# Optimization experiments

Measured on AMD Instinct MI355X. Metric: run time of the kernel, lower is better.

Reference implementation:

```python
import jax, jax.numpy as jnp
import numpy as np

THR = 1.0                      # spike threshold
DECAY_V = float(np.exp(-1.0 / 20.0))
GAMMA = 0.3                    # surrogate-gradient dampening factor
OUT_DECAY = 0.8                # exp_convolve decay

@jax.custom_vjp
def spike_fn(v_scaled):
    # Heaviside spike with pseudo-derivative gamma*max(0, 1-|v_scaled|)
    return (v_scaled > 0.0).astype(v_scaled.dtype)

def _spike_fwd(v_scaled):
    return spike_fn(v_scaled), v_scaled

def _spike_bwd(v_scaled, g):
    return (g * GAMMA * jnp.maximum(0.0, 1.0 - jnp.abs(v_scaled)),)

spike_fn.defvjp(_spike_fwd, _spike_bwd)


def setup_inputs() -> dict:
    key = jax.random.key(0)
    k1, k2, k3, k4 = jax.random.split(key, 4)
    B, T, NI, NR = 32, 1000, 128, 512
    inputs = jax.random.normal(k1, (B, T, NI), dtype=jnp.float32)
    w_in = jax.random.normal(k2, (NI, NR), dtype=jnp.float32) / np.sqrt(NI)
    w_rec = jax.random.normal(k3, (NR, NR), dtype=jnp.float32) / np.sqrt(NR)
    w_out = jax.random.normal(k4, (NR, 1), dtype=jnp.float32) / np.sqrt(NR)
    b_out = jnp.zeros((1,), dtype=jnp.float32)
    return {"inputs": inputs, "w_in": w_in, "w_rec": w_rec, "w_out": w_out, "b_out": b_out}


def reference(inputs, w_in, w_rec, w_out, b_out):
    B, T, _ = inputs.shape
    NR = w_rec.shape[0]
    dtype = inputs.dtype
    # no autapses (zero diagonal on recurrent weights, as in LSNN cells)
    w_rec_masked = w_rec * (1.0 - jnp.eye(NR, dtype=dtype))
    # precompute feedforward input currents: [T, B, NR]
    i_in = jnp.swapaxes(jnp.einsum('bti,iu->btu', inputs, w_in), 0, 1)

    def lif_step(carry, x_t):
        v, z = carry
        i_t = x_t + z @ w_rec_masked           # [B, NR]
        v_new = DECAY_V * v + i_t - z * THR    # reset by subtraction
        z_new = spike_fn((v_new - THR) / THR)
        return (v_new, z_new), (v_new, z_new)

    v0 = jnp.zeros((B, NR), dtype)
    z0 = jnp.zeros((B, NR), dtype)
    _, (vs, zs) = jax.lax.scan(lif_step, (v0, z0), i_in)
    voltages = jnp.swapaxes(vs, 0, 1)  # [B, T, NR]
    spikes = jnp.swapaxes(zs, 0, 1)    # [B, T, NR]

    proj = spikes @ w_out + b_out      # [B, T, 1]

    def filt_step(a, x):
        a_new = OUT_DECAY * a + (1.0 - OUT_DECAY) * x
        return a_new, a_new

    f0 = jnp.zeros((B, 1), dtype)
    _, pred = jax.lax.scan(filt_step, f0, jnp.swapaxes(proj, 0, 1))
    prediction = jnp.swapaxes(pred, 0, 1)  # [B, T, 1]
    return voltages, spikes, prediction
```

## Files before the change

kernel.cpp:

```cpp
#include <hip/hip_runtime.h>

#define NR 512
#define NI 128
#define B 32
#define T 1000
#define G 32

__device__ __forceinline__ float mul_nofma(float a, float b) {
    float r = a * b;
    asm volatile("" : "+v"(r));
    return r;
}

__device__ __forceinline__ void bar_lds() {
    asm volatile("s_waitcnt lgkmcnt(0)\n\ts_barrier" ::: "memory");
}

__global__ __launch_bounds__(512) void k_prep(const float* __restrict__ w_rec,
                                              float* __restrict__ w_ws) {
    const int r = blockIdx.x, u = threadIdx.x;
    float val = 0.f;
    if (r < NR && r != u) val = w_rec[r * NR + u];
    w_ws[r * NR + u] = val;
}

template <int ROWS>
__global__ __launch_bounds__(512) void k_in_gemm(const float* __restrict__ inputs,
                                                 const float* __restrict__ w_in,
                                                 float* __restrict__ i_in) {
    const int u = threadIdx.x;
    const int r0 = blockIdx.x * ROWS;
    float acc[ROWS];
#pragma unroll
    for (int r = 0; r < ROWS; ++r) acc[r] = 0.f;
    const float* __restrict__ inp = inputs + (long)r0 * NI;
#pragma unroll 4
    for (int i = 0; i < NI; ++i) {
        float w = w_in[i * NR + u];
#pragma unroll
        for (int r = 0; r < ROWS; ++r)
            acc[r] = __builtin_fmaf(inp[r * NI + i], w, acc[r]);
    }
#pragma unroll
    for (int r = 0; r < ROWS; ++r)
        i_in[(long)(r0 + r) * NR + u] = acc[r];
}

__device__ __forceinline__ void loadg1(float (&buf)[G], const int* __restrict__ lp,
                                       const float* __restrict__ w_ws, int u) {
#pragma unroll
    for (int qq = 0; qq < G / 4; ++qq) {
        int4 jv = *(const int4*)(lp + qq * 4);
        int j0 = __builtin_amdgcn_readfirstlane(jv.x);
        int j1 = __builtin_amdgcn_readfirstlane(jv.y);
        int j2 = __builtin_amdgcn_readfirstlane(jv.z);
        int j3 = __builtin_amdgcn_readfirstlane(jv.w);
        buf[qq * 4 + 0] = w_ws[j0 * NR + u];
        buf[qq * 4 + 1] = w_ws[j1 * NR + u];
        buf[qq * 4 + 2] = w_ws[j2 * NR + u];
        buf[qq * 4 + 3] = w_ws[j3 * NR + u];
    }
}

__device__ __forceinline__ void sumg1(const float (&buf)[G], float& s) {
#pragma unroll
    for (int q = 0; q < G; ++q) s = __fadd_rn(s, buf[q]);
}

__global__ __launch_bounds__(1024) void k_scan(const float* __restrict__ w_ws,
                                               float* __restrict__ out) {
    const int b = blockIdx.x;
    const int tid = threadIdx.x;
    const int u = tid & (NR - 1);
    const int h = tid >> 9;
    const int wav = tid >> 6;
    const int lane = tid & 63;

    float* __restrict__ volt_b = out + (long)b * (T * NR);
    float* __restrict__ spk_b  = out + (long)B * T * NR + (long)b * (T * NR);

    __shared__ __align__(16) int listA[256];
    __shared__ __align__(16) int listB[256];
    __shared__ int wcnt[8];
    __shared__ float shs[2][NR];

    float v = 0.f, z = 0.f;
    const float decay = 0.951229424500714f;
    __syncthreads();

    for (int t = 0; t < T; ++t) {
        float ii = volt_b[t * NR + u];

        unsigned long long m = __ballot(z > 0.5f);
        if (h == 0 && lane == 0) wcnt[wav] = __popcll(m);
        bar_lds();

        const int c0 = wcnt[0], c1 = wcnt[1], c2 = wcnt[2], c3 = wcnt[3];
        const int c4 = wcnt[4], c5 = wcnt[5], c6 = wcnt[6], c7 = wcnt[7];
        const int cnt_lo = c0 + c1 + c2 + c3;
        const int cnt_hi = c4 + c5 + c6 + c7;

        if (h == 0) {
            if (z > 0.5f) {
                int below = __popcll(m & ((1ull << lane) - 1ull));
                if (wav < 4) {
                    int pos = (wav > 0 ? c0 : 0) + (wav > 1 ? c1 : 0) + (wav > 2 ? c2 : 0) + below;
                    listA[pos] = u;
                } else {
                    int pos = (wav > 4 ? c4 : 0) + (wav > 5 ? c5 : 0) + (wav > 6 ? c6 : 0) + below;
                    listB[pos] = u;
                }
            }
            if (u < 256) { if (u >= cnt_lo) listA[u] = NR; }
            else         { int x = u - 256; if (x >= cnt_hi) listB[x] = NR; }
        }
        bar_lds();

        const int* lp  = h ? listB : listA;
        const int  myn = h ? ((cnt_hi + G - 1) / G) : ((cnt_lo + G - 1) / G);
        float s = 0.f;
        if (myn > 0) {
            float bA[G], bB[G];
            loadg1(bA, lp, w_ws, u);
            int g = 0;
            while (true) {
                if (g + 1 < myn) loadg1(bB, lp + (g + 1) * G, w_ws, u);
                sumg1(bA, s);
                ++g;
                if (g == myn) break;
                if (g + 1 < myn) loadg1(bA, lp + (g + 1) * G, w_ws, u);
                sumg1(bB, s);
                ++g;
                if (g == myn) break;
            }
        }
        shs[h][u] = s;
        bar_lds();

        float rec = __fadd_rn(shs[0][u], shs[1][u]);
        float it = __fadd_rn(ii, rec);
        float m1 = mul_nofma(decay, v);
        float t2 = __fadd_rn(m1, it);
        float vn = __fsub_rn(t2, z);
        float zn = (vn > 1.0f) ? 1.0f : 0.0f;
        if (h == 0) {
            volt_b[t * NR + u] = vn;
            spk_b[t * NR + u]  = zn;
        }
        v = vn; z = zn;
    }
}

__global__ __launch_bounds__(512) void k_pred(const float* __restrict__ w_out,
                                              const float* __restrict__ b_out,
                                              float* __restrict__ out) {
    const int b = blockIdx.x;
    const int tid = threadIdx.x;
    const int wav = tid >> 6, lane = tid & 63;
    const float* __restrict__ spk_b = out + (long)B * T * NR + (long)b * (T * NR);
    float* __restrict__ pred = out + 2L * B * T * NR + (long)b * T;

    __shared__ double projs[T];

    double wo[8];
#pragma unroll
    for (int q = 0; q < 8; ++q) wo[q] = (double)w_out[lane + q * 64];

    for (int t = wav; t < T; t += 8) {
        double p = 0.0;
#pragma unroll
        for (int q = 0; q < 8; ++q)
            p += (double)spk_b[t * NR + lane + q * 64] * wo[q];
#pragma unroll
        for (int o = 32; o > 0; o >>= 1) p += __shfl_xor(p, o, 64);
        if (lane == 0) projs[t] = p;
    }
    __syncthreads();
    if (tid == 0) {
        const double bo = (double)b_out[0];
        double ema = 0.0;
        for (int t = 0; t < T; ++t) {
            ema = 0.8 * ema + 0.2 * (bo + projs[t]);
            pred[t] = (float)ema;
        }
    }
}

__global__ __launch_bounds__(512) void k_scan_ref(const float* __restrict__ w_rec,
                                                  const float* __restrict__ w_out,
                                                  const float* __restrict__ b_out,
                                                  float* __restrict__ out) {
    const int b = blockIdx.x;
    const int u = threadIdx.x;
    const int wav = u >> 6, lane = u & 63;
    const int KC = 256;

    float* __restrict__ volt_b = out + (long)b * (T * NR);
    float* __restrict__ spk_b  = out + (long)B * T * NR + (long)b * (T * NR);
    float* __restrict__ pred   = out + 2L * B * T * NR;

    __shared__ __align__(16) int list[NR];
    __shared__ int wcnt[8];
    __shared__ double projp[8];

    float v = 0.f, z = 0.f;
    const float decay = 0.951229424500714f;
    const double wo = (double)w_out[u];
    const double bo = (double)b_out[0];
    double ema = 0.0;

    for (int t = 0; t < T; ++t) {
        unsigned long long m = __ballot(z > 0.5f);
        if (lane == 0) wcnt[wav] = __popcll(m);
        __syncthreads();
        int cnt = 0, base = 0;
#pragma unroll
        for (int w2 = 0; w2 < 8; ++w2) {
            int c = wcnt[w2];
            if (w2 < wav) base += c;
            cnt += c;
        }
        if (z > 0.5f) {
            int pos = base + __popcll(m & ((1ull << lane) - 1ull));
            list[pos] = u;
        }
        float ii = volt_b[t * NR + u];
        __syncthreads();

        float s1 = 0.f, s2 = 0.f;
        int k = 0;
        for (; k + 8 <= cnt; k += 8) {
            int4 ja = *(const int4*)&list[k];
            int4 jb = *(const int4*)&list[k + 4];
            int j0 = __builtin_amdgcn_readfirstlane(ja.x);
            int j1 = __builtin_amdgcn_readfirstlane(ja.y);
            int j2 = __builtin_amdgcn_readfirstlane(ja.z);
            int j3 = __builtin_amdgcn_readfirstlane(ja.w);
            int j4 = __builtin_amdgcn_readfirstlane(jb.x);
            int j5 = __builtin_amdgcn_readfirstlane(jb.y);
            int j6 = __builtin_amdgcn_readfirstlane(jb.z);
            int j7 = __builtin_amdgcn_readfirstlane(jb.w);
            float w0 = w_rec[j0 * NR + u]; if (j0 == u) w0 = 0.f;
            float w1 = w_rec[j1 * NR + u]; if (j1 == u) w1 = 0.f;
            float w2 = w_rec[j2 * NR + u]; if (j2 == u) w2 = 0.f;
            float w3 = w_rec[j3 * NR + u]; if (j3 == u) w3 = 0.f;
            float w4 = w_rec[j4 * NR + u]; if (j4 == u) w4 = 0.f;
            float w5 = w_rec[j5 * NR + u]; if (j5 == u) w5 = 0.f;
            float w6 = w_rec[j6 * NR + u]; if (j6 == u) w6 = 0.f;
            float w7 = w_rec[j7 * NR + u]; if (j7 == u) w7 = 0.f;
            if (j0 < KC) s1 = __fadd_rn(s1, w0); else s2 = __fadd_rn(s2, w0);
            if (j1 < KC) s1 = __fadd_rn(s1, w1); else s2 = __fadd_rn(s2, w1);
            if (j2 < KC) s1 = __fadd_rn(s1, w2); else s2 = __fadd_rn(s2, w2);
            if (j3 < KC) s1 = __fadd_rn(s1, w3); else s2 = __fadd_rn(s2, w3);
            if (j4 < KC) s1 = __fadd_rn(s1, w4); else s2 = __fadd_rn(s2, w4);
            if (j5 < KC) s1 = __fadd_rn(s1, w5); else s2 = __fadd_rn(s2, w5);
            if (j6 < KC) s1 = __fadd_rn(s1, w6); else s2 = __fadd_rn(s2, w6);
            if (j7 < KC) s1 = __fadd_rn(s1, w7); else s2 = __fadd_rn(s2, w7);
        }
        for (; k < cnt; ++k) {
            int j = __builtin_amdgcn_readfirstlane(list[k]);
            float w = w_rec[j * NR + u];
            if (j == u) w = 0.f;
            if (j < KC) s1 = __fadd_rn(s1, w); else s2 = __fadd_rn(s2, w);
        }
        float rec = __fadd_rn(s1, s2);

        float it = __fadd_rn(ii, rec);
        float m1 = mul_nofma(decay, v);
        float t2 = __fadd_rn(m1, it);
        float vn = __fsub_rn(t2, z);
        float zn = (vn > 1.0f) ? 1.0f : 0.0f;
        volt_b[t * NR + u] = vn;
        spk_b[t * NR + u]  = zn;

        double p = (double)zn * wo;
#pragma unroll
        for (int o = 32; o > 0; o >>= 1) p += __shfl_xor(p, o, 64);
        if (lane == 0) projp[wav] = p;
        __syncthreads();
        if (u == 0) {
            double pr = bo;
#pragma unroll
            for (int w2 = 0; w2 < 8; ++w2) pr += projp[w2];
            ema = 0.8 * ema + 0.2 * pr;
            pred[b * T + t] = (float)ema;
        }
        v = vn; z = zn;
    }
}

extern "C" void kernel_launch(void* const* d_in, const int* in_sizes, int n_in,
                              void* d_out, int out_size, void* d_ws, size_t ws_size,
                              hipStream_t stream) {
    const float* inputs = (const float*)d_in[0];
    const float* w_in   = (const float*)d_in[1];
    const float* w_rec  = (const float*)d_in[2];
    const float* w_out  = (const float*)d_in[3];
    const float* b_out  = (const float*)d_in[4];
    float* out = (float*)d_out;

    k_in_gemm<16><<<dim3(B * T / 16), dim3(512), 0, stream>>>(inputs, w_in, out);

    const size_t need = (size_t)(NR + 1) * NR * sizeof(float);
    if (ws_size >= need) {
        float* w_ws = (float*)d_ws;
        k_prep<<<dim3(NR + 1), dim3(512), 0, stream>>>(w_rec, w_ws);
        k_scan<<<dim3(B), dim3(1024), 0, stream>>>(w_ws, out);
        k_pred<<<dim3(B), dim3(512), 0, stream>>>(w_out, b_out, out);
    } else {
        k_scan_ref<<<dim3(B), dim3(512), 0, stream>>>(w_rec, w_out, b_out, out);
    }
}
```

Baseline: 2.184 ms.

## Use per-wave spike list segments to drop a barrier per timestep

Each wave now writes its spiking indices into its own fixed 64-slot segment and pads the rest, so the global prefix sum over wave counts and its separate barrier are gone. The gather-sum then walks each wave segment in 16-wide chunks instead of double-buffered 32-wide groups over one compacted list. Only the upper half writes its partial to LDS, and the lower half finishes the update from its register. This cuts one barrier per timestep at the cost of extra padded loads per segment and less load pipelining. The summation order changes, which could perturb rounding near the threshold.

```diff
diff --git a/kernel.cpp b/kernel.cpp
--- a/kernel.cpp
+++ b/kernel.cpp
@@ -4,7 +4,6 @@
 #define NI 128
 #define B 32
 #define T 1000
-#define G 32
 
 __device__ __forceinline__ float mul_nofma(float a, float b) {
     float r = a * b;
@@ -46,25 +45,41 @@
         i_in[(long)(r0 + r) * NR + u] = acc[r];
 }
 
-__device__ __forceinline__ void loadg1(float (&buf)[G], const int* __restrict__ lp,
-                                       const float* __restrict__ w_ws, int u) {
-#pragma unroll
-    for (int qq = 0; qq < G / 4; ++qq) {
-        int4 jv = *(const int4*)(lp + qq * 4);
-        int j0 = __builtin_amdgcn_readfirstlane(jv.x);
-        int j1 = __builtin_amdgcn_readfirstlane(jv.y);
-        int j2 = __builtin_amdgcn_readfirstlane(jv.z);
-        int j3 = __builtin_amdgcn_readfirstlane(jv.w);
-        buf[qq * 4 + 0] = w_ws[j0 * NR + u];
-        buf[qq * 4 + 1] = w_ws[j1 * NR + u];
-        buf[qq * 4 + 2] = w_ws[j2 * NR + u];
-        buf[qq * 4 + 3] = w_ws[j3 * NR + u];
-    }
-}
-
-__device__ __forceinline__ void sumg1(const float (&buf)[G], float& s) {
-#pragma unroll
-    for (int q = 0; q < G; ++q) s = __fadd_rn(s, buf[q]);
+__device__ __forceinline__ void sum16(const int* __restrict__ sp,
+                                      const float* __restrict__ w_ws, int u,
+                                      float& s) {
+    int4 ja = *(const int4*)(sp);
+    int4 jb = *(const int4*)(sp + 4);
+    int4 jc = *(const int4*)(sp + 8);
+    int4 jd = *(const int4*)(sp + 12);
+    const float* r0  = w_ws + (__builtin_amdgcn_readfirstlane(ja.x) << 9);
+    const float* r1  = w_ws + (__builtin_amdgcn_readfirstlane(ja.y) << 9);
+    const float* r2  = w_ws + (__builtin_amdgcn_readfirstlane(ja.z) << 9);
+    const float* r3  = w_ws + (__builtin_amdgcn_readfirstlane(ja.w) << 9);
+    const float* r4  = w_ws + (__builtin_amdgcn_readfirstlane(jb.x) << 9);
+    const float* r5  = w_ws + (__builtin_amdgcn_readfirstlane(jb.y) << 9);
+    const float* r6  = w_ws + (__builtin_amdgcn_readfirstlane(jb.z) << 9);
+    const float* r7  = w_ws + (__builtin_amdgcn_readfirstlane(jb.w) << 9);
+    const float* r8  = w_ws + (__builtin_amdgcn_readfirstlane(jc.x) << 9);
+    const float* r9  = w_ws + (__builtin_amdgcn_readfirstlane(jc.y) << 9);
+    const float* r10 = w_ws + (__builtin_amdgcn_readfirstlane(jc.z) << 9);
+    const float* r11 = w_ws + (__builtin_amdgcn_readfirstlane(jc.w) << 9);
+    const float* r12 = w_ws + (__builtin_amdgcn_readfirstlane(jd.x) << 9);
+    const float* r13 = w_ws + (__builtin_amdgcn_readfirstlane(jd.y) << 9);
+    const float* r14 = w_ws + (__builtin_amdgcn_readfirstlane(jd.z) << 9);
+    const float* r15 = w_ws + (__builtin_amdgcn_readfirstlane(jd.w) << 9);
+    float f0 = r0[u], f1 = r1[u], f2 = r2[u], f3 = r3[u];
+    float f4 = r4[u], f5 = r5[u], f6 = r6[u], f7 = r7[u];
+    float f8 = r8[u], f9 = r9[u], f10 = r10[u], f11 = r11[u];
+    float f12 = r12[u], f13 = r13[u], f14 = r14[u], f15 = r15[u];
+    s = __fadd_rn(s, f0);  s = __fadd_rn(s, f1);
+    s = __fadd_rn(s, f2);  s = __fadd_rn(s, f3);
+    s = __fadd_rn(s, f4);  s = __fadd_rn(s, f5);
+    s = __fadd_rn(s, f6);  s = __fadd_rn(s, f7);
+    s = __fadd_rn(s, f8);  s = __fadd_rn(s, f9);
+    s = __fadd_rn(s, f10); s = __fadd_rn(s, f11);
+    s = __fadd_rn(s, f12); s = __fadd_rn(s, f13);
+    s = __fadd_rn(s, f14); s = __fadd_rn(s, f15);
 }
 
 __global__ __launch_bounds__(1024) void k_scan(const float* __restrict__ w_ws,
@@ -81,73 +96,56 @@
 
     __shared__ __align__(16) int listA[256];
     __shared__ __align__(16) int listB[256];
-    __shared__ int wcnt[8];
-    __shared__ float shs[2][NR];
+    __shared__ __align__(16) int wcnt8[8];
+    __shared__ float shs1[NR];
 
     float v = 0.f, z = 0.f;
     const float decay = 0.951229424500714f;
-    __syncthreads();
 
     for (int t = 0; t < T; ++t) {
-        float ii = volt_b[t * NR + u];
-
-        unsigned long long m = __ballot(z > 0.5f);
-        if (h == 0 && lane == 0) wcnt[wav] = __popcll(m);
-        bar_lds();
-
-        const int c0 = wcnt[0], c1 = wcnt[1], c2 = wcnt[2], c3 = wcnt[3];
-        const int c4 = wcnt[4], c5 = wcnt[5], c6 = wcnt[6], c7 = wcnt[7];
-        const int cnt_lo = c0 + c1 + c2 + c3;
-        const int cnt_hi = c4 + c5 + c6 + c7;
-
+        float ii = 0.f;
         if (h == 0) {
+            ii = volt_b[t * NR + u];
+
+            unsigned long long m = __ballot(z > 0.5f);
+            int myc = __popcll(m);
+            int* seg = (wav < 4) ? (listA + wav * 64) : (listB + (wav - 4) * 64);
             if (z > 0.5f) {
                 int below = __popcll(m & ((1ull << lane) - 1ull));
-                if (wav < 4) {
-                    int pos = (wav > 0 ? c0 : 0) + (wav > 1 ? c1 : 0) + (wav > 2 ? c2 : 0) + below;
-                    listA[pos] = u;
-                } else {
-                    int pos = (wav > 4 ? c4 : 0) + (wav > 5 ? c5 : 0) + (wav > 6 ? c6 : 0) + below;
-                    listB[pos] = u;
-                }
+                seg[below] = u;
             }
-            if (u < 256) { if (u >= cnt_lo) listA[u] = NR; }
-            else         { int x = u - 256; if (x >= cnt_hi) listB[x] = NR; }
+            if (lane >= myc) seg[lane] = NR;
+            if (lane == 0) wcnt8[wav] = myc;
         }
         bar_lds();
 
-        const int* lp  = h ? listB : listA;
-        const int  myn = h ? ((cnt_hi + G - 1) / G) : ((cnt_lo + G - 1) / G);
         float s = 0.f;
-        if (myn > 0) {
-            float bA[G], bB[G];
-            loadg1(bA, lp, w_ws, u);
-            int g = 0;
-            while (true) {
-                if (g + 1 < myn) loadg1(bB, lp + (g + 1) * G, w_ws, u);
-                sumg1(bA, s);
-                ++g;
-                if (g == myn) break;
-                if (g + 1 < myn) loadg1(bA, lp + (g + 1) * G, w_ws, u);
-                sumg1(bB, s);
-                ++g;
-                if (g == myn) break;
+        {
+            const int* lp = h ? listB : listA;
+            int4 cq = *(const int4*)&wcnt8[h * 4];
+#pragma unroll
+            for (int w = 0; w < 4; ++w) {
+                int c = (w == 0) ? cq.x : (w == 1) ? cq.y : (w == 2) ? cq.z : cq.w;
+                int pc = (c + 15) & ~15;
+                const int* sp = lp + w * 64;
+                for (int k = 0; k < pc; k += 16)
+                    sum16(sp + k, w_ws, u, s);
             }
         }
-        shs[h][u] = s;
+        if (h == 1) shs1[u] = s;
         bar_lds();
 
-        float rec = __fadd_rn(shs[0][u], shs[1][u]);
-        float it = __fadd_rn(ii, rec);
-        float m1 = mul_nofma(decay, v);
-        float t2 = __fadd_rn(m1, it);
-        float vn = __fsub_rn(t2, z);
-        float zn = (vn > 1.0f) ? 1.0f : 0.0f;
         if (h == 0) {
+            float rec = __fadd_rn(s, shs1[u]);
+            float it = __fadd_rn(ii, rec);
+            float m1 = mul_nofma(decay, v);
+            float t2 = __fadd_rn(m1, it);
+            float vn = __fsub_rn(t2, z);
+            float zn = (vn > 1.0f) ? 1.0f : 0.0f;
             volt_b[t * NR + u] = vn;
             spk_b[t * NR + u]  = zn;
-        }
-        v = vn; z = zn;
+            v = vn; z = zn;
+        }
     }
 }
 
```

Result: slower. 2.964 ms (+35.7%).
